# Kernel tuning notes

Hardware: AMD Instinct MI355X
Metric: run time of the kernel (lower is better)

## Reference

```python
import jax, jax.numpy as jnp
import numpy as np

M, N, D, H, R = 16384, 32, 128, 8, 237
Dh = D // H
SCALE = Dh ** -0.5
LN_EPS = 1e-5


def setup_inputs() -> dict:
    key = jax.random.key(0)
    ks = jax.random.split(key, 12)
    entity_repr = jax.random.normal(ks[0], (M, D), dtype=jnp.float32)
    neighbor_index = jax.random.randint(ks[1], (M, N), 0, M, dtype=jnp.int64)
    rel_ids = jax.random.randint(ks[2], (M, N), 0, R, dtype=jnp.int64)
    neighbor_mask = jax.random.randint(ks[3], (M, N), 0, 2, dtype=jnp.int32).astype(bool)
    neighbor_mask = neighbor_mask.at[:, 0].set(True)  # ensure >=1 valid neighbor per node
    s = 1.0 / np.sqrt(D)
    # weights stored in right-multiply form: y = x @ W + b
    Wq = jax.random.normal(ks[4], (D, D), dtype=jnp.float32) * s
    Wk = jax.random.normal(ks[5], (D, D), dtype=jnp.float32) * s
    Wv = jax.random.normal(ks[6], (D, D), dtype=jnp.float32) * s
    Wo = jax.random.normal(ks[7], (D, D), dtype=jnp.float32) * s
    bq = jnp.zeros((D,), jnp.float32)
    bk = jnp.zeros((D,), jnp.float32)
    bv = jnp.zeros((D,), jnp.float32)
    bo = jnp.zeros((D,), jnp.float32)
    rel_table = jax.random.normal(ks[8], (R, D), dtype=jnp.float32)
    ln_gamma = jnp.ones((D,), jnp.float32)
    ln_beta = jnp.zeros((D,), jnp.float32)
    return {
        "entity_repr": entity_repr, "neighbor_index": neighbor_index,
        "rel_ids": rel_ids, "neighbor_mask": neighbor_mask,
        "Wq": Wq, "bq": bq, "Wk": Wk, "bk": bk, "Wv": Wv, "bv": bv,
        "Wo": Wo, "bo": bo, "rel_table": rel_table,
        "ln_gamma": ln_gamma, "ln_beta": ln_beta,
    }


def _layernorm(x, gamma, beta):
    mu = jnp.mean(x, axis=-1, keepdims=True)
    var = jnp.var(x, axis=-1, keepdims=True)
    return (x - mu) * jax.lax.rsqrt(var + LN_EPS) * gamma + beta


def reference(entity_repr, neighbor_index, rel_ids, neighbor_mask,
              Wq, bq, Wk, bk, Wv, bv, Wo, bo, rel_table, ln_gamma, ln_beta):
    valid = neighbor_mask
    safe_index = jnp.where(valid, neighbor_index, 0)
    safe_rel = jnp.where(valid, rel_ids, 0)
    neighbor_repr = entity_repr[safe_index]          # [M, N, D] irregular gather
    rel_emb = rel_table[safe_rel]                     # [M, N, D]
    q = (entity_repr @ Wq + bq).reshape(M, H, Dh)     # [M, H, Dh] (query len 1)
    k = ((neighbor_repr + rel_emb) @ Wk + bk).reshape(M, N, H, Dh)
    v = (neighbor_repr @ Wv + bv).reshape(M, N, H, Dh)
    attn = jnp.einsum("mhd,mnhd->mhn", q, k) * SCALE  # [M, H, N]
    attn = jnp.where(valid[:, None, :], attn, -jnp.inf)
    attn = jax.nn.softmax(attn, axis=-1)
    attn = jnp.nan_to_num(attn, nan=0.0)
    out = jnp.einsum("mhn,mnhd->mhd", attn, v).reshape(M, D)
    out = out @ Wo + bo
    return _layernorm(entity_repr + out, ln_gamma, ln_beta)
```

## Files before the change

### kernel.cpp

```cpp
#include <hip/hip_runtime.h>

#define M_NODES 16384
#define NNBR 32
#define RREL 237
#define ATTN_SCALE 0.25f
#define LN_EPS 1e-5f

typedef float float4v __attribute__((ext_vector_type(4)));
typedef unsigned int uint4v __attribute__((ext_vector_type(4)));
typedef short short8 __attribute__((ext_vector_type(8)));
typedef float floatx4 __attribute__((ext_vector_type(4)));

__device__ __forceinline__ float bfu2f(unsigned short u) {
    return __builtin_bit_cast(float, ((unsigned int)u) << 16);
}
__device__ __forceinline__ unsigned short f2bfu(float f) {
    unsigned int x = __builtin_bit_cast(unsigned int, f);
    unsigned int lsb = (x >> 16) & 1u;
    x += 0x7fffu + lsb;
    return (unsigned short)(x >> 16);
}
__device__ __forceinline__ unsigned int pack2(float a, float b) {
    return (unsigned int)f2bfu(a) | ((unsigned int)f2bfu(b) << 16);
}
__device__ __forceinline__ float unpk_lo(unsigned int u) {
    return __builtin_bit_cast(float, u << 16);
}
__device__ __forceinline__ float unpk_hi(unsigned int u) {
    return __builtin_bit_cast(float, u & 0xffff0000u);
}


__global__ __launch_bounds__(256) void prep_w(
    const float* __restrict__ Wq, const float* __restrict__ Wk,
    const float* __restrict__ Wv, const float* __restrict__ Wo,
    unsigned short* __restrict__ WqT, unsigned short* __restrict__ WkT,
    unsigned short* __restrict__ WvT, unsigned short* __restrict__ WoT) {
    int mat  = blockIdx.x >> 3;
    int slab = blockIdx.x & 7;
    const float* W = (mat == 0) ? Wq : (mat == 1) ? Wk : (mat == 2) ? Wv : Wo;
    unsigned short* WT = (mat == 0) ? WqT : (mat == 1) ? WkT : (mat == 2) ? WvT : WoT;
    int t = threadIdx.x;
    #pragma unroll
    for (int i = 0; i < 8; ++i) {
        int idx = t + 256 * i;
        int r = slab * 16 + (idx >> 7);
        int c = idx & 127;
        WT[c * 128 + r] = f2bfu(W[r * 128 + c]);
    }
}

__global__ __launch_bounds__(256) void gemm4_mfma(
    const float* __restrict__ entity, const float* __restrict__ rel_table,
    const unsigned short* __restrict__ WqT, const unsigned short* __restrict__ WkT,
    const unsigned short* __restrict__ WvT,
    const float* __restrict__ bq, const float* __restrict__ bk,
    const float* __restrict__ bv,
    unsigned short* __restrict__ EQb, unsigned short* __restrict__ EKV,
    unsigned short* __restrict__ RKb) {
    __shared__ __align__(16) unsigned short lw[128 * 136];

    int y = blockIdx.y;
    const float* A; const unsigned short* WT; const float* bias; int arows;
    unsigned short* outb; int ostride, ooff;
    if (y == 0)      { A = entity;    WT = WqT; bias = bq;      arows = M_NODES; outb = EQb; ostride = 128; ooff = 0;   }
    else if (y == 1) { A = entity;    WT = WkT; bias = nullptr; arows = M_NODES; outb = EKV; ostride = 256; ooff = 0;   }
    else if (y == 2) { A = entity;    WT = WvT; bias = bv;      arows = M_NODES; outb = EKV; ostride = 256; ooff = 128; }
    else             { A = rel_table; WT = WkT; bias = bk;      arows = RREL;    outb = RKb; ostride = 128; ooff = 0;   }

    int rbase = blockIdx.x * 64;
    if (rbase >= arows) return;
    int t = threadIdx.x;

    #pragma unroll
    for (int i = 0; i < 8; ++i) {
        int ci = t + 256 * i;
        int r  = ci >> 4;
        int c8 = ci & 15;
        *(short8*)&lw[r * 136 + c8 * 8] = *(const short8*)&WT[r * 128 + c8 * 8];
    }
    __syncthreads();

    int wave = t >> 6, lane = t & 63;
    int lm = lane & 15, quad = lane >> 4;
    int m0 = rbase + wave * 16;

    floatx4 acc[8];
    #pragma unroll
    for (int c = 0; c < 8; ++c) acc[c] = (floatx4){0.f, 0.f, 0.f, 0.f};

    int r0 = m0 + lm; if (r0 >= arows) r0 = arows - 1;

    #pragma unroll
    for (int ks = 0; ks < 4; ++ks) {
        int koff = ks * 32 + quad * 8;
        float4v f0 = *(const float4v*)&A[r0 * 128 + koff];
        float4v f1 = *(const float4v*)&A[r0 * 128 + koff + 4];
        short8 a;
        #pragma unroll
        for (int j = 0; j < 4; ++j) {
            a[j]     = (short)f2bfu(f0[j]);
            a[4 + j] = (short)f2bfu(f1[j]);
        }
        #pragma unroll
        for (int c = 0; c < 8; ++c) {
            short8 b = *(const short8*)&lw[(c * 16 + lm) * 136 + koff];
            acc[c] = __builtin_amdgcn_mfma_f32_16x16x32_bf16(a, b, acc[c], 0, 0, 0);
        }
    }

    #pragma unroll
    for (int c = 0; c < 8; ++c) {
        int col = c * 16 + lm;
        float bb = bias ? bias[col] : 0.0f;
        int rb = m0 + quad * 4;
        #pragma unroll
        for (int j = 0; j < 4; ++j) {
            int r = rb + j;
            if (r < arows) outb[r * ostride + ooff + col] = f2bfu(acc[c][j] + bb);
        }
    }
}

__global__ __launch_bounds__(256) void attn_gather(
    const int* __restrict__ nidx, const int* __restrict__ nrel,
    const int* __restrict__ nmask,
    const unsigned short* __restrict__ EQb, const unsigned short* __restrict__ EKV,
    const unsigned short* __restrict__ RKb,
    unsigned short* __restrict__ OATb) {
    __shared__ float Pl[4][8][33];
    __shared__ int mix[4][32];
    __shared__ int mrl[4][32];

    int w = threadIdx.x >> 6, l = threadIdx.x & 63;
    int m = blockIdx.x * 4 + w;
    int lm = l & 15, quad = l >> 4;
    int n0 = l & 31;

    int mk = nmask[m * NNBR + n0];
    int ix = nidx[m * NNBR + n0];
    int ir = nrel[m * NNBR + n0];
    if (!mk) { ix = 0; ir = 0; }
    ix = ix < 0 ? 0 : (ix > M_NODES - 1 ? M_NODES - 1 : ix);
    ir = ir < 0 ? 0 : (ir > RREL - 1 ? RREL - 1 : ir);
    unsigned long long bal = __ballot(mk != 0);
    unsigned maskbits = (unsigned)(bal & 0xffffffffu);
    if (l < 32) { mix[w][l] = ix; mrl[w][l] = ir; }

    short8 vreg[8];
    #pragma unroll
    for (int i = 0; i < 8; ++i) {
        int ixx = mix[w][quad + i * 4];
        vreg[i] = *(const short8*)&EKV[ixx * 256 + 128 + lm * 8];
    }

    int rowK0 = mix[w][lm],      rowK1 = mix[w][16 + lm];
    int rowR0 = mrl[w][lm],      rowR1 = mrl[w][16 + lm];

    floatx4 acc0 = (floatx4){0.f, 0.f, 0.f, 0.f};
    floatx4 acc1 = (floatx4){0.f, 0.f, 0.f, 0.f};
    const short8 zero8 = (short8){0, 0, 0, 0, 0, 0, 0, 0};
    #pragma unroll
    for (int ks = 0; ks < 4; ++ks) {
        int koff = ks * 32 + quad * 8;
        short8 q8 = *(const short8*)&EQb[m * 128 + koff];
        int h = ks * 2 + (quad >> 1);
        short8 bq = (lm == h) ? q8 : zero8;
        short8 k0 = *(const short8*)&EKV[rowK0 * 256 + koff];
        short8 k1 = *(const short8*)&EKV[rowK1 * 256 + koff];
        short8 r0 = *(const short8*)&RKb[rowR0 * 128 + koff];
        short8 r1 = *(const short8*)&RKb[rowR1 * 128 + koff];
        acc0 = __builtin_amdgcn_mfma_f32_16x16x32_bf16(k0, bq, acc0, 0, 0, 0);
        acc0 = __builtin_amdgcn_mfma_f32_16x16x32_bf16(r0, bq, acc0, 0, 0, 0);
        acc1 = __builtin_amdgcn_mfma_f32_16x16x32_bf16(k1, bq, acc1, 0, 0, 0);
        acc1 = __builtin_amdgcn_mfma_f32_16x16x32_bf16(r1, bq, acc1, 0, 0, 0);
    }

    float lf[2][4];
    #pragma unroll
    for (int j = 0; j < 4; ++j) {
        int na = quad * 4 + j, nb = 16 + quad * 4 + j;
        float va = acc0[j] * ATTN_SCALE;
        float vb = acc1[j] * ATTN_SCALE;
        lf[0][j] = ((maskbits >> na) & 1) ? va : -1e30f;
        lf[1][j] = ((maskbits >> nb) & 1) ? vb : -1e30f;
    }
    float mx = -1e30f;
    #pragma unroll
    for (int g = 0; g < 2; ++g)
        #pragma unroll
        for (int j = 0; j < 4; ++j) mx = fmaxf(mx, lf[g][j]);
    mx = fmaxf(mx, __shfl_xor(mx, 16, 64));
    mx = fmaxf(mx, __shfl_xor(mx, 32, 64));
    float p[2][4];
    float s = 0.f;
    #pragma unroll
    for (int g = 0; g < 2; ++g)
        #pragma unroll
        for (int j = 0; j < 4; ++j) { p[g][j] = __expf(lf[g][j] - mx); s += p[g][j]; }
    s += __shfl_xor(s, 16, 64);
    s += __shfl_xor(s, 32, 64);
    float inv = 1.0f / s;
    if (lm < 8) {
        #pragma unroll
        for (int g = 0; g < 2; ++g)
            #pragma unroll
            for (int j = 0; j < 4; ++j)
                Pl[w][lm][g * 16 + quad * 4 + j] = p[g][j] * inv;
    }

    float o[8] = {0.f, 0.f, 0.f, 0.f, 0.f, 0.f, 0.f, 0.f};
    #pragma unroll
    for (int i = 0; i < 8; ++i) {
        float pp = Pl[w][lm >> 1][quad + i * 4];
        #pragma unroll
        for (int j = 0; j < 8; ++j) o[j] += pp * bfu2f((unsigned short)vreg[i][j]);
    }
    #pragma unroll
    for (int j = 0; j < 8; ++j) {
        o[j] += __shfl_xor(o[j], 16, 64);
        o[j] += __shfl_xor(o[j], 32, 64);
    }
    if (quad == 0) {
        uint4v u;
        u[0] = pack2(o[0], o[1]); u[1] = pack2(o[2], o[3]);
        u[2] = pack2(o[4], o[5]); u[3] = pack2(o[6], o[7]);
        *(uint4v*)&OATb[m * 128 + lm * 8] = u;
    }
}

__global__ __launch_bounds__(128) void gemm_wo_ln(
    const unsigned short* __restrict__ OATb, const unsigned short* __restrict__ WoT,
    const float* __restrict__ bo, const float* __restrict__ entity,
    const float* __restrict__ gamma_, const float* __restrict__ beta_,
    float* __restrict__ OUT) {
    __shared__ __align__(16) unsigned short lw[128 * 136];

    int t = threadIdx.x;
    #pragma unroll
    for (int i = 0; i < 16; ++i) {
        int ci = t + 128 * i;
        int r  = ci >> 4;
        int c8 = ci & 15;
        *(short8*)&lw[r * 136 + c8 * 8] = *(const short8*)&WoT[r * 128 + c8 * 8];
    }
    __syncthreads();

    int wave = t >> 6, lane = t & 63;
    int lm = lane & 15, quad = lane >> 4;
    int rbase = blockIdx.x * 64;
    int m0 = rbase + wave * 32;

    floatx4 acc[2][8];
    #pragma unroll
    for (int i = 0; i < 2; ++i)
        #pragma unroll
        for (int c = 0; c < 8; ++c) acc[i][c] = (floatx4){0.f, 0.f, 0.f, 0.f};

    int r0 = m0 + lm, r1 = m0 + 16 + lm;
    #pragma unroll
    for (int ks = 0; ks < 4; ++ks) {
        int koff = ks * 32 + quad * 8;
        short8 a0 = *(const short8*)&OATb[r0 * 128 + koff];
        short8 a1 = *(const short8*)&OATb[r1 * 128 + koff];
        #pragma unroll
        for (int c = 0; c < 8; ++c) {
            short8 b = *(const short8*)&lw[(c * 16 + lm) * 136 + koff];
            acc[0][c] = __builtin_amdgcn_mfma_f32_16x16x32_bf16(a0, b, acc[0][c], 0, 0, 0);
            acc[1][c] = __builtin_amdgcn_mfma_f32_16x16x32_bf16(a1, b, acc[1][c], 0, 0, 0);
        }
    }

    float bb[8], gg[8], be[8];
    #pragma unroll
    for (int c = 0; c < 8; ++c) {
        int col = c * 16 + lm;
        bb[c] = bo[col]; gg[c] = gamma_[col]; be[c] = beta_[col];
    }
    #pragma unroll
    for (int i = 0; i < 2; ++i) {
        #pragma unroll
        for (int j = 0; j < 4; ++j) {
            int r = m0 + i * 16 + quad * 4 + j;
            float y[8];
            float s1 = 0.f, s2 = 0.f;
            #pragma unroll
            for (int c = 0; c < 8; ++c) {
                float v = acc[i][c][j] + bb[c] + entity[r * 128 + c * 16 + lm];
                y[c] = v; s1 += v; s2 += v * v;
            }
            #pragma unroll
            for (int off = 8; off >= 1; off >>= 1) {
                s1 += __shfl_xor(s1, off, 16);
                s2 += __shfl_xor(s2, off, 16);
            }
            float mu  = s1 * (1.0f / 128.0f);
            float var = fmaxf(s2 * (1.0f / 128.0f) - mu * mu, 0.0f);
            float rs  = rsqrtf(var + LN_EPS);
            #pragma unroll
            for (int c = 0; c < 8; ++c)
                OUT[r * 128 + c * 16 + lm] = (y[c] - mu) * rs * gg[c] + be[c];
        }
    }
}

__global__ __launch_bounds__(256, 6) void rga_fused(
    const float* __restrict__ entity,
    const int* __restrict__ nidx,
    const int* __restrict__ nrel,
    const int* __restrict__ nmask,
    const float* __restrict__ Wq, const float* __restrict__ bq,
    const float* __restrict__ Wk, const float* __restrict__ bk,
    const float* __restrict__ Wv, const float* __restrict__ bv,
    const float* __restrict__ Wo, const float* __restrict__ bo,
    const float* __restrict__ rel_table,
    const float* __restrict__ gamma_, const float* __restrict__ beta_,
    float* __restrict__ outp) {
    __shared__ __align__(16) float er[128];
    __shared__ __align__(16) float qv[128];
    __shared__ float qb[8];
    __shared__ __align__(16) float qk[8 * 132];
    __shared__ __align__(16) unsigned int nbvp[32 * 68];
    __shared__ float Lg[8][33];
    __shared__ __align__(16) float pv[8 * 132];
    __shared__ __align__(16) float oat[128];
    __shared__ float ypart[2][128];
    __shared__ float red[4];
    __shared__ int midx[32], mrel[32], mmask[32];

    int m = blockIdx.x;
    int t = threadIdx.x;

    if (t < 32) {
        int mk = nmask[m * NNBR + t];
        int ix = nidx[m * NNBR + t];
        int ir = nrel[m * NNBR + t];
        if (!mk) { ix = 0; ir = 0; }
        ix = ix < 0 ? 0 : (ix > M_NODES - 1 ? M_NODES - 1 : ix);
        ir = ir < 0 ? 0 : (ir > RREL - 1 ? RREL - 1 : ir);
        mmask[t] = mk; midx[t] = ix; mrel[t] = ir;
    }
    if (t >= 128) er[t - 128] = entity[m * 128 + (t - 128)];
    __syncthreads();

    {
        int half = t >> 7, d = t & 127, j0 = half * 64;
        const float4v* e4 = (const float4v*)&er[j0];
        float acc = 0.f;
        #pragma unroll 4
        for (int c = 0; c < 16; ++c) {
            float4v ev = e4[c];
            #pragma unroll
            for (int k = 0; k < 4; ++k)
                acc += ev[k] * Wq[(j0 + c * 4 + k) * 128 + d];
        }
        ypart[half][d] = acc;
    }
    __syncthreads();
    if (t < 128) qv[t] = ypart[0][t] + ypart[1][t] + bq[t];
    __syncthreads();

    #pragma unroll
    for (int rep = 0; rep < 4; ++rep) {
        int o = rep * 256 + t;
        int h = o >> 7, j = o & 127;
        const float4v* wr = (const float4v*)&Wk[j * 128 + h * 16];
        const float4v* q4 = (const float4v*)&qv[h * 16];
        float s = 0.f;
        #pragma unroll
        for (int c = 0; c < 4; ++c) {
            float4v ww = wr[c], q = q4[c];
            #pragma unroll
            for (int k = 0; k < 4; ++k) s += ww[k] * q[k];
        }
        qk[h * 132 + j] = s;
    }
    if (t < 8) {
        float s = 0.f;
        #pragma unroll
        for (int dh = 0; dh < 16; ++dh) s += qv[t * 16 + dh] * bk[t * 16 + dh];
        qb[t] = s;
    }
    __syncthreads();

    {
        int n = t >> 3, c16 = t & 7, j0 = c16 * 16;
        int ix = midx[n], ir = mrel[n];
        const float4v* ep = (const float4v*)&entity[ix * 128 + j0];
        const float4v* rp = (const float4v*)&rel_table[ir * 128 + j0];
        float ev[16], kv[16];
        #pragma unroll
        for (int c = 0; c < 4; ++c) {
            float4v e4 = ep[c], r4 = rp[c];
            #pragma unroll
            for (int k = 0; k < 4; ++k) {
                ev[c * 4 + k] = e4[k];
                kv[c * 4 + k] = e4[k] + r4[k];
            }
        }
        uint4v u0, u1;
        #pragma unroll
        for (int k = 0; k < 4; ++k) u0[k] = pack2(ev[2 * k], ev[2 * k + 1]);
        #pragma unroll
        for (int k = 0; k < 4; ++k) u1[k] = pack2(ev[8 + 2 * k], ev[9 + 2 * k]);
        *(uint4v*)&nbvp[n * 68 + c16 * 8]     = u0;
        *(uint4v*)&nbvp[n * 68 + c16 * 8 + 4] = u1;
        float acc[8];
        #pragma unroll
        for (int h = 0; h < 8; ++h) {
            const float4v* qrow = (const float4v*)&qk[h * 132 + j0];
            float s = 0.f;
            #pragma unroll
            for (int c = 0; c < 4; ++c) {
                float4v q = qrow[c];
                #pragma unroll
                for (int k = 0; k < 4; ++k) s += q[k] * kv[c * 4 + k];
            }
            acc[h] = s;
        }
        #pragma unroll
        for (int off = 1; off < 8; off <<= 1) {
            #pragma unroll
            for (int h = 0; h < 8; ++h) acc[h] += __shfl_xor(acc[h], off, 8);
        }
        if (c16 == 0) {
            #pragma unroll
            for (int h = 0; h < 8; ++h) {
                float lf = (acc[h] + qb[h]) * ATTN_SCALE;
                if (!mmask[n]) lf = -1e30f;
                Lg[h][n] = lf;
            }
        }
    }
    __syncthreads();

    {
        int h = t >> 5, n = t & 31;
        float lf = Lg[h][n];
        float mx = lf;
        #pragma unroll
        for (int off = 16; off >= 1; off >>= 1) mx = fmaxf(mx, __shfl_xor(mx, off, 32));
        float p = __expf(lf - mx);
        float s = p;
        #pragma unroll
        for (int off = 16; off >= 1; off >>= 1) s += __shfl_xor(s, off, 32);
        Lg[h][n] = p / s;
    }
    __syncthreads();

    {
        int h = t >> 5, c4 = t & 31;
        float4v a = (float4v){0.f, 0.f, 0.f, 0.f};
        #pragma unroll 8
        for (int n = 0; n < 32; ++n) {
            float p = Lg[h][n];
            unsigned int w0 = nbvp[n * 68 + c4 * 2];
            unsigned int w1 = nbvp[n * 68 + c4 * 2 + 1];
            a[0] += p * unpk_lo(w0);
            a[1] += p * unpk_hi(w0);
            a[2] += p * unpk_lo(w1);
            a[3] += p * unpk_hi(w1);
        }
        *(float4v*)&pv[h * 132 + c4 * 4] = a;
    }
    __syncthreads();

    {
        int half = t >> 7, d = t & 127, j0 = half * 64;
        int h = d >> 4;
        const float4v* p4 = (const float4v*)&pv[h * 132 + j0];
        float acc = 0.f;
        #pragma unroll 4
        for (int c = 0; c < 16; ++c) {
            float4v p = p4[c];
            #pragma unroll
            for (int k = 0; k < 4; ++k)
                acc += p[k] * Wv[(j0 + c * 4 + k) * 128 + d];
        }
        ypart[half][d] = acc;
    }
    __syncthreads();
    if (t < 128) oat[t] = ypart[0][t] + ypart[1][t] + bv[t];
    __syncthreads();

    {
        int half = t >> 7, d = t & 127, j0 = half * 64;
        const float4v* o4 = (const float4v*)&oat[j0];
        float acc = 0.f;
        #pragma unroll 4
        for (int c = 0; c < 16; ++c) {
            float4v o = o4[c];
            #pragma unroll
            for (int k = 0; k < 4; ++k)
                acc += o[k] * Wo[(j0 + c * 4 + k) * 128 + d];
        }
        ypart[half][d] = acc;
    }
    __syncthreads();

    float x = 0.f;
    if (t < 128) {
        x = er[t] + ypart[0][t] + ypart[1][t] + bo[t];
        float s1 = x, s2 = x * x;
        #pragma unroll
        for (int off = 32; off >= 1; off >>= 1) {
            s1 += __shfl_xor(s1, off, 64);
            s2 += __shfl_xor(s2, off, 64);
        }
        if ((t & 63) == 0) { red[(t >> 6) * 2] = s1; red[(t >> 6) * 2 + 1] = s2; }
    }
    __syncthreads();
    if (t < 128) {
        float mu  = (red[0] + red[2]) * (1.0f / 128.0f);
        float ms  = (red[1] + red[3]) * (1.0f / 128.0f);
        float var = fmaxf(ms - mu * mu, 0.0f);
        float rs  = rsqrtf(var + LN_EPS);
        outp[m * 128 + t] = (x - mu) * rs * gamma_[t] + beta_[t];
    }
}

extern "C" void kernel_launch(void* const* d_in, const int* in_sizes, int n_in,
                              void* d_out, int out_size, void* d_ws, size_t ws_size,
                              hipStream_t stream) {
    const float* entity    = (const float*)d_in[0];
    const int*   nidx      = (const int*)d_in[1];
    const int*   nrel      = (const int*)d_in[2];
    const int*   nmask     = (const int*)d_in[3];
    const float* Wq        = (const float*)d_in[4];
    const float* bq        = (const float*)d_in[5];
    const float* Wk        = (const float*)d_in[6];
    const float* bk        = (const float*)d_in[7];
    const float* Wv        = (const float*)d_in[8];
    const float* bv        = (const float*)d_in[9];
    const float* Wo        = (const float*)d_in[10];
    const float* bo        = (const float*)d_in[11];
    const float* rel_table = (const float*)d_in[12];
    const float* gamma_    = (const float*)d_in[13];
    const float* beta_     = (const float*)d_in[14];

    char* ws = (char*)d_ws;
    unsigned short* EKV  = (unsigned short*)(ws + 0);
    unsigned short* EQb  = (unsigned short*)(ws + 8388608);
    unsigned short* OATb = (unsigned short*)(ws + 12582912);
    unsigned short* RKb  = (unsigned short*)(ws + 16777216);
    unsigned short* WqT  = (unsigned short*)(ws + 16837888);
    unsigned short* WkT  = (unsigned short*)(ws + 16870656);
    unsigned short* WvT  = (unsigned short*)(ws + 16903424);
    unsigned short* WoT  = (unsigned short*)(ws + 16936192);
    const size_t NEED = 16968960;

    if (ws_size >= NEED) {
        prep_w<<<dim3(32), 256, 0, stream>>>(Wq, Wk, Wv, Wo, WqT, WkT, WvT, WoT);
        gemm4_mfma<<<dim3(256, 4), 256, 0, stream>>>(
            entity, rel_table, WqT, WkT, WvT, bq, bk, bv, EQb, EKV, RKb);
        attn_gather<<<dim3(M_NODES / 4), 256, 0, stream>>>(
            nidx, nrel, nmask, EQb, EKV, RKb, OATb);
        gemm_wo_ln<<<dim3(256), 128, 0, stream>>>(
            OATb, WoT, bo, entity, gamma_, beta_, (float*)d_out);
    } else {
        rga_fused<<<dim3(M_NODES), 256, 0, stream>>>(
            entity, nidx, nrel, nmask, Wq, bq, Wk, bk, Wv, bv, Wo, bo,
            rel_table, gamma_, beta_, (float*)d_out);
    }
}
```

Measured before the change: 143.4 us.

## Pre-convert entity to bf16, hoist A-fragment loads, shuffle indices, widen Wo GEMM

The entity matrix is converted to bf16 once in the prep kernel, so the three projection GEMMs read half the bytes and skip repeated fp32-to-bf16 conversion. A-operand fragments are loaded before the LDS weight staging so their latency overlaps it. In attn_gather, neighbor indices are broadcast with wave shuffles instead of an LDS round trip, and the query fragments are loaded up front. gemm_wo_ln moves to 256 threads with 16 rows per wave. In exchange this adds a 4MB workspace buffer and an extra pass over entity.

```diff
diff --git a/kernel.cpp b/kernel.cpp
--- a/kernel.cpp
+++ b/kernel.cpp
@@ -34,24 +34,45 @@
 __global__ __launch_bounds__(256) void prep_w(
     const float* __restrict__ Wq, const float* __restrict__ Wk,
     const float* __restrict__ Wv, const float* __restrict__ Wo,
+    const float* __restrict__ entity,
     unsigned short* __restrict__ WqT, unsigned short* __restrict__ WkT,
-    unsigned short* __restrict__ WvT, unsigned short* __restrict__ WoT) {
-    int mat  = blockIdx.x >> 3;
-    int slab = blockIdx.x & 7;
-    const float* W = (mat == 0) ? Wq : (mat == 1) ? Wk : (mat == 2) ? Wv : Wo;
-    unsigned short* WT = (mat == 0) ? WqT : (mat == 1) ? WkT : (mat == 2) ? WvT : WoT;
+    unsigned short* __restrict__ WvT, unsigned short* __restrict__ WoT,
+    unsigned short* __restrict__ Eb) {
     int t = threadIdx.x;
-    #pragma unroll
-    for (int i = 0; i < 8; ++i) {
-        int idx = t + 256 * i;
-        int r = slab * 16 + (idx >> 7);
-        int c = idx & 127;
-        WT[c * 128 + r] = f2bfu(W[r * 128 + c]);
+    if (blockIdx.x < 32) {
+        int mat  = blockIdx.x >> 3;
+        int slab = blockIdx.x & 7;
+        const float* W = (mat == 0) ? Wq : (mat == 1) ? Wk : (mat == 2) ? Wv : Wo;
+        unsigned short* WT = (mat == 0) ? WqT : (mat == 1) ? WkT : (mat == 2) ? WvT : WoT;
+        #pragma unroll
+        for (int i = 0; i < 8; ++i) {
+            int idx = t + 256 * i;
+            int r = slab * 16 + (idx >> 7);
+            int c = idx & 127;
+            WT[c * 128 + r] = f2bfu(W[r * 128 + c]);
+        }
+    } else {
+        int b = blockIdx.x - 32;
+        const float* src = entity + (size_t)b * 16384;
+        unsigned short* dst = Eb + (size_t)b * 16384;
+        #pragma unroll
+        for (int i = 0; i < 8; ++i) {
+            int o = (i * 256 + t) * 8;
+            float4v f0 = *(const float4v*)&src[o];
+            float4v f1 = *(const float4v*)&src[o + 4];
+            short8 s;
+            #pragma unroll
+            for (int j = 0; j < 4; ++j) {
+                s[j]     = (short)f2bfu(f0[j]);
+                s[4 + j] = (short)f2bfu(f1[j]);
+            }
+            *(short8*)&dst[o] = s;
+        }
     }
 }
 
 __global__ __launch_bounds__(256) void gemm4_mfma(
-    const float* __restrict__ entity, const float* __restrict__ rel_table,
+    const float* __restrict__ rel_table, const unsigned short* __restrict__ Eb,
     const unsigned short* __restrict__ WqT, const unsigned short* __restrict__ WkT,
     const unsigned short* __restrict__ WvT,
     const float* __restrict__ bq, const float* __restrict__ bk,
@@ -61,16 +82,39 @@
     __shared__ __align__(16) unsigned short lw[128 * 136];
 
     int y = blockIdx.y;
-    const float* A; const unsigned short* WT; const float* bias; int arows;
+    const unsigned short* WT; const float* bias; int arows;
     unsigned short* outb; int ostride, ooff;
-    if (y == 0)      { A = entity;    WT = WqT; bias = bq;      arows = M_NODES; outb = EQb; ostride = 128; ooff = 0;   }
-    else if (y == 1) { A = entity;    WT = WkT; bias = nullptr; arows = M_NODES; outb = EKV; ostride = 256; ooff = 0;   }
-    else if (y == 2) { A = entity;    WT = WvT; bias = bv;      arows = M_NODES; outb = EKV; ostride = 256; ooff = 128; }
-    else             { A = rel_table; WT = WkT; bias = bk;      arows = RREL;    outb = RKb; ostride = 128; ooff = 0;   }
+    if (y == 0)      { WT = WqT; bias = bq;      arows = M_NODES; outb = EQb; ostride = 128; ooff = 0;   }
+    else if (y == 1) { WT = WkT; bias = nullptr; arows = M_NODES; outb = EKV; ostride = 256; ooff = 0;   }
+    else if (y == 2) { WT = WvT; bias = bv;      arows = M_NODES; outb = EKV; ostride = 256; ooff = 128; }
+    else             { WT = WkT; bias = bk;      arows = RREL;    outb = RKb; ostride = 128; ooff = 0;   }
 
     int rbase = blockIdx.x * 64;
     if (rbase >= arows) return;
     int t = threadIdx.x;
+    int wave = t >> 6, lane = t & 63;
+    int lm = lane & 15, quad = lane >> 4;
+    int m0 = rbase + wave * 16;
+    int r0 = m0 + lm; if (r0 >= arows) r0 = arows - 1;
+
+    short8 af[4];
+    if (y == 3) {
+        #pragma unroll
+        for (int ks = 0; ks < 4; ++ks) {
+            int koff = ks * 32 + quad * 8;
+            float4v f0 = *(const float4v*)&rel_table[r0 * 128 + koff];
+            float4v f1 = *(const float4v*)&rel_table[r0 * 128 + koff + 4];
+            #pragma unroll
+            for (int j = 0; j < 4; ++j) {
+                af[ks][j]     = (short)f2bfu(f0[j]);
+                af[ks][4 + j] = (short)f2bfu(f1[j]);
+            }
+        }
+    } else {
+        #pragma unroll
+        for (int ks = 0; ks < 4; ++ks)
+            af[ks] = *(const short8*)&Eb[r0 * 128 + ks * 32 + quad * 8];
+    }
 
     #pragma unroll
     for (int i = 0; i < 8; ++i) {
@@ -81,31 +125,17 @@
     }
     __syncthreads();
 
-    int wave = t >> 6, lane = t & 63;
-    int lm = lane & 15, quad = lane >> 4;
-    int m0 = rbase + wave * 16;
-
     floatx4 acc[8];
     #pragma unroll
     for (int c = 0; c < 8; ++c) acc[c] = (floatx4){0.f, 0.f, 0.f, 0.f};
-
-    int r0 = m0 + lm; if (r0 >= arows) r0 = arows - 1;
 
     #pragma unroll
     for (int ks = 0; ks < 4; ++ks) {
         int koff = ks * 32 + quad * 8;
-        float4v f0 = *(const float4v*)&A[r0 * 128 + koff];
-        float4v f1 = *(const float4v*)&A[r0 * 128 + koff + 4];
-        short8 a;
-        #pragma unroll
-        for (int j = 0; j < 4; ++j) {
-            a[j]     = (short)f2bfu(f0[j]);
-            a[4 + j] = (short)f2bfu(f1[j]);
-        }
         #pragma unroll
         for (int c = 0; c < 8; ++c) {
             short8 b = *(const short8*)&lw[(c * 16 + lm) * 136 + koff];
-            acc[c] = __builtin_amdgcn_mfma_f32_16x16x32_bf16(a, b, acc[c], 0, 0, 0);
+            acc[c] = __builtin_amdgcn_mfma_f32_16x16x32_bf16(af[ks], b, acc[c], 0, 0, 0);
         }
     }
 
@@ -129,13 +159,16 @@
     const unsigned short* __restrict__ RKb,
     unsigned short* __restrict__ OATb) {
     __shared__ float Pl[4][8][33];
-    __shared__ int mix[4][32];
-    __shared__ int mrl[4][32];
 
     int w = threadIdx.x >> 6, l = threadIdx.x & 63;
     int m = blockIdx.x * 4 + w;
     int lm = l & 15, quad = l >> 4;
     int n0 = l & 31;
+
+    short8 q8v[4];
+    #pragma unroll
+    for (int ks = 0; ks < 4; ++ks)
+        q8v[ks] = *(const short8*)&EQb[m * 128 + ks * 32 + quad * 8];
 
     int mk = nmask[m * NNBR + n0];
     int ix = nidx[m * NNBR + n0];
@@ -145,17 +178,16 @@
     ir = ir < 0 ? 0 : (ir > RREL - 1 ? RREL - 1 : ir);
     unsigned long long bal = __ballot(mk != 0);
     unsigned maskbits = (unsigned)(bal & 0xffffffffu);
-    if (l < 32) { mix[w][l] = ix; mrl[w][l] = ir; }
 
     short8 vreg[8];
     #pragma unroll
     for (int i = 0; i < 8; ++i) {
-        int ixx = mix[w][quad + i * 4];
+        int ixx = __shfl(ix, quad + i * 4, 64);
         vreg[i] = *(const short8*)&EKV[ixx * 256 + 128 + lm * 8];
     }
 
-    int rowK0 = mix[w][lm],      rowK1 = mix[w][16 + lm];
-    int rowR0 = mrl[w][lm],      rowR1 = mrl[w][16 + lm];
+    int rowK0 = __shfl(ix, lm, 64),      rowK1 = __shfl(ix, 16 + lm, 64);
+    int rowR0 = __shfl(ir, lm, 64),      rowR1 = __shfl(ir, 16 + lm, 64);
 
     floatx4 acc0 = (floatx4){0.f, 0.f, 0.f, 0.f};
     floatx4 acc1 = (floatx4){0.f, 0.f, 0.f, 0.f};
@@ -163,9 +195,8 @@
     #pragma unroll
     for (int ks = 0; ks < 4; ++ks) {
         int koff = ks * 32 + quad * 8;
-        short8 q8 = *(const short8*)&EQb[m * 128 + koff];
         int h = ks * 2 + (quad >> 1);
-        short8 bq = (lm == h) ? q8 : zero8;
+        short8 bq = (lm == h) ? q8v[ks] : zero8;
         short8 k0 = *(const short8*)&EKV[rowK0 * 256 + koff];
         short8 k1 = *(const short8*)&EKV[rowK1 * 256 + koff];
         short8 r0 = *(const short8*)&RKb[rowR0 * 128 + koff];
@@ -229,7 +260,7 @@
     }
 }
 
-__global__ __launch_bounds__(128) void gemm_wo_ln(
+__global__ __launch_bounds__(256) void gemm_wo_ln(
     const unsigned short* __restrict__ OATb, const unsigned short* __restrict__ WoT,
     const float* __restrict__ bo, const float* __restrict__ entity,
     const float* __restrict__ gamma_, const float* __restrict__ beta_,
@@ -237,37 +268,36 @@
     __shared__ __align__(16) unsigned short lw[128 * 136];
 
     int t = threadIdx.x;
-    #pragma unroll
-    for (int i = 0; i < 16; ++i) {
-        int ci = t + 128 * i;
+    int wave = t >> 6, lane = t & 63;
+    int lm = lane & 15, quad = lane >> 4;
+    int m0 = blockIdx.x * 64 + wave * 16;
+    int r0 = m0 + lm;
+
+    short8 af[4];
+    #pragma unroll
+    for (int ks = 0; ks < 4; ++ks)
+        af[ks] = *(const short8*)&OATb[r0 * 128 + ks * 32 + quad * 8];
+
+    #pragma unroll
+    for (int i = 0; i < 8; ++i) {
+        int ci = t + 256 * i;
         int r  = ci >> 4;
         int c8 = ci & 15;
         *(short8*)&lw[r * 136 + c8 * 8] = *(const short8*)&WoT[r * 128 + c8 * 8];
     }
     __syncthreads();
 
-    int wave = t >> 6, lane = t & 63;
-    int lm = lane & 15, quad = lane >> 4;
-    int rbase = blockIdx.x * 64;
-    int m0 = rbase + wave * 32;
-
-    floatx4 acc[2][8];
-    #pragma unroll
-    for (int i = 0; i < 2; ++i)
-        #pragma unroll
-        for (int c = 0; c < 8; ++c) acc[i][c] = (floatx4){0.f, 0.f, 0.f, 0.f};
-
-    int r0 = m0 + lm, r1 = m0 + 16 + lm;
+    floatx4 acc[8];
+    #pragma unroll
+    for (int c = 0; c < 8; ++c) acc[c] = (floatx4){0.f, 0.f, 0.f, 0.f};
+
     #pragma unroll
     for (int ks = 0; ks < 4; ++ks) {
         int koff = ks * 32 + quad * 8;
-        short8 a0 = *(const short8*)&OATb[r0 * 128 + koff];
-        short8 a1 = *(const short8*)&OATb[r1 * 128 + koff];
         #pragma unroll
         for (int c = 0; c < 8; ++c) {
             short8 b = *(const short8*)&lw[(c * 16 + lm) * 136 + koff];
-            acc[0][c] = __builtin_amdgcn_mfma_f32_16x16x32_bf16(a0, b, acc[0][c], 0, 0, 0);
-            acc[1][c] = __builtin_amdgcn_mfma_f32_16x16x32_bf16(a1, b, acc[1][c], 0, 0, 0);
+            acc[c] = __builtin_amdgcn_mfma_f32_16x16x32_bf16(af[ks], b, acc[c], 0, 0, 0);
         }
     }
 
@@ -278,29 +308,26 @@
         bb[c] = bo[col]; gg[c] = gamma_[col]; be[c] = beta_[col];
     }
     #pragma unroll
-    for (int i = 0; i < 2; ++i) {
-        #pragma unroll
-        for (int j = 0; j < 4; ++j) {
-            int r = m0 + i * 16 + quad * 4 + j;
-            float y[8];
-            float s1 = 0.f, s2 = 0.f;
-            #pragma unroll
-            for (int c = 0; c < 8; ++c) {
-                float v = acc[i][c][j] + bb[c] + entity[r * 128 + c * 16 + lm];
-                y[c] = v; s1 += v; s2 += v * v;
-            }
-            #pragma unroll
-            for (int off = 8; off >= 1; off >>= 1) {
-                s1 += __shfl_xor(s1, off, 16);
-                s2 += __shfl_xor(s2, off, 16);
-            }
-            float mu  = s1 * (1.0f / 128.0f);
-            float var = fmaxf(s2 * (1.0f / 128.0f) - mu * mu, 0.0f);
-            float rs  = rsqrtf(var + LN_EPS);
-            #pragma unroll
-            for (int c = 0; c < 8; ++c)
-                OUT[r * 128 + c * 16 + lm] = (y[c] - mu) * rs * gg[c] + be[c];
-        }
+    for (int j = 0; j < 4; ++j) {
+        int r = m0 + quad * 4 + j;
+        float y[8];
+        float s1 = 0.f, s2 = 0.f;
+        #pragma unroll
+        for (int c = 0; c < 8; ++c) {
+            float v = acc[c][j] + bb[c] + entity[r * 128 + c * 16 + lm];
+            y[c] = v; s1 += v; s2 += v * v;
+        }
+        #pragma unroll
+        for (int off = 8; off >= 1; off >>= 1) {
+            s1 += __shfl_xor(s1, off, 16);
+            s2 += __shfl_xor(s2, off, 16);
+        }
+        float mu  = s1 * (1.0f / 128.0f);
+        float var = fmaxf(s2 * (1.0f / 128.0f) - mu * mu, 0.0f);
+        float rs  = rsqrtf(var + LN_EPS);
+        #pragma unroll
+        for (int c = 0; c < 8; ++c)
+            OUT[r * 128 + c * 16 + lm] = (y[c] - mu) * rs * gg[c] + be[c];
     }
 }
 
@@ -547,15 +574,17 @@
     unsigned short* WkT  = (unsigned short*)(ws + 16870656);
     unsigned short* WvT  = (unsigned short*)(ws + 16903424);
     unsigned short* WoT  = (unsigned short*)(ws + 16936192);
-    const size_t NEED = 16968960;
+    unsigned short* Eb   = (unsigned short*)(ws + 16968960);
+    const size_t NEED = 16968960 + 4194304;
 
     if (ws_size >= NEED) {
-        prep_w<<<dim3(32), 256, 0, stream>>>(Wq, Wk, Wv, Wo, WqT, WkT, WvT, WoT);
+        prep_w<<<dim3(160), 256, 0, stream>>>(Wq, Wk, Wv, Wo, entity,
+                                              WqT, WkT, WvT, WoT, Eb);
         gemm4_mfma<<<dim3(256, 4), 256, 0, stream>>>(
-            entity, rel_table, WqT, WkT, WvT, bq, bk, bv, EQb, EKV, RKb);
+            rel_table, Eb, WqT, WkT, WvT, bq, bk, bv, EQb, EKV, RKb);
         attn_gather<<<dim3(M_NODES / 4), 256, 0, stream>>>(
             nidx, nrel, nmask, EQb, EKV, RKb, OATb);
-        gemm_wo_ln<<<dim3(256), 128, 0, stream>>>(
+        gemm_wo_ln<<<dim3(256), 256, 0, stream>>>(
             OATb, WoT, bo, entity, gamma_, beta_, (float*)d_out);
     } else {
         rga_fused<<<dim3(M_NODES), 256, 0, stream>>>(
```

New measurement: 137.5 us. 1.04x faster.
